# Optimization experiments

Hardware: AMD Instinct MI355X
Metric: run time of the kernel (lower is better)

Reference implementation:

```python
import jax, jax.numpy as jnp
import numpy as np

B, LC, LQ = 16, 512, 64
H = 256            # args.hidden_dim (BiLSTM output dim)
D = 4 * H          # feedforward / biaffine input dim
DFF = 512          # args.hidden_dim_ffw
C = 3              # num_labels


def setup_inputs() -> dict:
    key = jax.random.key(0)
    ks = jax.random.split(key, 12)
    sc = 0.02
    return {
        "ctx_emb": jax.random.normal(ks[0], (B, LC, H), jnp.float32),
        "ques_emb": jax.random.normal(ks[1], (B, LQ, H), jnp.float32),
        "w_sim": jax.random.normal(ks[2], (3 * H,), jnp.float32) * sc,
        "W1s": jax.random.normal(ks[3], (D, DFF), jnp.float32) * sc,
        "b1s": jnp.zeros((DFF,), jnp.float32),
        "W2s": jax.random.normal(ks[4], (DFF, D), jnp.float32) * sc,
        "b2s": jnp.zeros((D,), jnp.float32),
        "W1e": jax.random.normal(ks[5], (D, DFF), jnp.float32) * sc,
        "b1e": jnp.zeros((DFF,), jnp.float32),
        "W2e": jax.random.normal(ks[6], (DFF, D), jnp.float32) * sc,
        "b2e": jnp.zeros((D,), jnp.float32),
        "Wb": jax.random.normal(ks[7], (D + 1, C, D + 1), jnp.float32) * sc,
    }


def _ffw(x, W1, b1, W2, b2):
    # FeedforwardLayer: w_2(relu(w_1(x))) (dropout is identity at eval)
    return jnp.maximum(x @ W1 + b1, 0.0) @ W2 + b2


def reference(ctx_emb, ques_emb, w_sim, W1s, b1s, W2s, b2s, W1e, b1e, W2e, b2e, Wb):
    w1, w2, w3 = jnp.split(w_sim, 3)
    # Fused BiDAF trilinear similarity: identical math to
    # Linear(cat([ctx_, ques_, ctx_*ques_], -1)) with weight [w1|w2|w3].
    sim = (ctx_emb @ w1)[:, :, None] + (ques_emb @ w2)[:, None, :] \
        + jnp.einsum('bih,bjh->bij', ctx_emb * w3, ques_emb)      # [B,LC,LQ]
    a = jax.nn.softmax(sim, axis=-1)                               # [B,LC,LQ]
    c2q = jnp.einsum('bij,bjh->bih', a, ques_emb)                  # [B,LC,H]
    b = jax.nn.softmax(jnp.max(sim, axis=2), axis=-1)              # [B,LC]
    q2c = jnp.einsum('bi,bih->bh', b, ctx_emb)[:, None, :]         # [B,1,H] broadcast over LC
    x = jnp.concatenate([ctx_emb, c2q, ctx_emb * c2q, ctx_emb * q2c], axis=2)  # [B,LC,4H]
    start = _ffw(x, W1s, b1s, W2s, b2s)                            # [B,LC,D]
    end = _ffw(x, W1e, b1e, W2e, b2e)                              # [B,LC,D]
    ones = jnp.ones(start.shape[:-1] + (1,), start.dtype)
    s1 = jnp.concatenate([start, ones], axis=-1)                   # [B,LC,D+1]
    e1 = jnp.concatenate([end, ones], axis=-1)                     # [B,LC,D+1]
    # Biaffine: score[b,x,y,c] = s1[b,x] . Wb[:,c,:] . e1[b,y]
    return jnp.einsum('bxi,icj,byj->bxyc', s1, Wb, e1)             # [B,LC,LC,C]
```

## Files before the change

### kernel.cpp

```cpp
#include <hip/hip_runtime.h>
#include <hip/hip_bf16.h>
#include <math.h>

typedef __bf16 bf16_t;
typedef bf16_t bf16x4 __attribute__((ext_vector_type(4)));
typedef bf16_t bf16x8 __attribute__((ext_vector_type(8)));
typedef float f32x4 __attribute__((ext_vector_type(4)));

#define Bsz 16
#define LCc 512
#define LQq 64
#define Hd 256
#define Dd 1024
#define DFFd 512
#define DP1 1025
#define KP 1152
#define NT 18
#define NIT 9
#define NP 1280
#define NROW 8192
#define YC 1536

#define OFF_T    0L
#define OFF_QW2  0L
#define OFF_MROW 4096L
#define OFF_Q2C  (OFF_MROW + 32768L)
#define OFF_C2Q  (OFF_Q2C + 16384L)
#define OFF_XB   (OFF_C2Q + 8388608L)
#define OFF_HBUF (OFF_XB + 16777216L)
#define OFF_W1ST (OFF_HBUF + 8388608L)
#define OFF_W2ST (OFF_W1ST + 1048576L)
#define OFF_W1ET (OFF_W2ST + 1048576L)
#define OFF_W2ET (OFF_W1ET + 1048576L)
#define OFF_S1   56623104L
#define OFF_E1   (OFF_S1 + 18874368L)
#define OFF_WBT  (OFF_E1 + 18874368L)

static __device__ __forceinline__ void gload_lds16(const void* g, void* l) {
    __builtin_amdgcn_global_load_lds(
        (const __attribute__((address_space(1))) void*)g,
        (__attribute__((address_space(3))) void*)l, 16, 0, 0);
}

__global__ __launch_bounds__(256) void k_qw2(const float* __restrict__ ques,
                                             const float* __restrict__ wsim,
                                             float* __restrict__ qw2) {
    int row = blockIdx.x * 4 + (threadIdx.x >> 6);
    int lane = threadIdx.x & 63;
    float4 q = *(const float4*)&ques[(long)row * Hd + lane * 4];
    float4 w = *(const float4*)&wsim[Hd + lane * 4];
    float p = q.x * w.x + q.y * w.y + q.z * w.z + q.w * w.w;
#pragma unroll
    for (int o = 32; o >= 1; o >>= 1) p += __shfl_xor(p, o, 64);
    if (lane == 0) qw2[row] = p;
}

__global__ __launch_bounds__(256) void k_wtrans(const float* __restrict__ in,
                                                bf16_t* __restrict__ out,
                                                int K, int N) {
    __shared__ float tile[32][33];
    int k0 = blockIdx.x * 32, n0 = blockIdx.y * 32;
    int r = threadIdx.x >> 5, c = threadIdx.x & 31;
#pragma unroll
    for (int rr = 0; rr < 32; rr += 8)
        tile[r + rr][c] = in[(long)(k0 + r + rr) * N + n0 + c];
    __syncthreads();
#pragma unroll
    for (int rr = 0; rr < 32; rr += 8)
        out[(long)(n0 + r + rr) * K + k0 + c] = (bf16_t)tile[c][r + rr];
}

__global__ __launch_bounds__(256) void k_wb(const float* __restrict__ Wb,
                                            bf16_t* __restrict__ Wbt) {
    int rowz = blockIdx.x;
    int c = rowz / NP, i = rowz % NP;
    int tid = threadIdx.x;
    bf16_t* orow = Wbt + (long)rowz * KP;
#pragma unroll
    for (int p = 0; p < 2; p++) {
        int j4 = tid + p * 256;
        if (j4 < KP / 4) {
            int j = j4 * 4;
            float x = 0.f, y = 0.f, z = 0.f, w = 0.f;
            if (i < DP1) {
                const float* src = Wb + ((long)i * 3 + c) * DP1 + j;
                if (j + 0 < DP1) x = src[0];
                if (j + 1 < DP1) y = src[1];
                if (j + 2 < DP1) z = src[2];
                if (j + 3 < DP1) w = src[3];
            }
            bf16x4 bv = {(bf16_t)x, (bf16_t)y, (bf16_t)z, (bf16_t)w};
            *(bf16x4*)&orow[j] = bv;
        }
    }
}

__global__ __launch_bounds__(256) void k_initse(bf16_t* __restrict__ s1,
                                                bf16_t* __restrict__ e1) {
    int idx = blockIdx.x * 256 + threadIdx.x;
    long r = idx >> 7; int cc = idx & 127;
    bf16_t v = (bf16_t)(cc == 0 ? 1.0f : 0.0f);
    s1[r * KP + 1024 + cc] = v;
    e1[r * KP + 1024 + cc] = v;
}

__global__ __launch_bounds__(256) void k_attn(const float* __restrict__ ctx,
                                              const float* __restrict__ ques,
                                              const float* __restrict__ wsim,
                                              const float* __restrict__ qw2,
                                              float* __restrict__ c2q,
                                              float* __restrict__ mrow) {
    __shared__ bf16x4 qlds[LQq * 64];
    __shared__ float cw3s[4][Hd];
    __shared__ float awave[4][LQq];
    int b = blockIdx.x >> 5;
    int itile = blockIdx.x & 31;
    int tid = threadIdx.x, wid = tid >> 6, lane = tid & 63;
#pragma unroll
    for (int p = 0; p < 16; p++) {
        int s = tid + p * 256;
        int j = s >> 6, h4s = s & 63;
        int h4 = h4s ^ (j & 15);
        float4 v = *(const float4*)&ques[((long)b * LQq + j) * Hd + h4 * 4];
        bf16x4 bv = {(bf16_t)v.x, (bf16_t)v.y, (bf16_t)v.z, (bf16_t)v.w};
        qlds[s] = bv;
    }
    float qw2r = qw2[b * LQq + lane];
    float4 w1v = *(const float4*)&wsim[lane * 4];
    float4 w3v = *(const float4*)&wsim[2 * Hd + lane * 4];
    __syncthreads();
    for (int rr = 0; rr < 4; rr++) {
        int i = itile * 16 + wid * 4 + rr;
        float4 cv = *(const float4*)&ctx[((long)b * LCc + i) * Hd + lane * 4];
        float cw1p = cv.x * w1v.x + cv.y * w1v.y + cv.z * w1v.z + cv.w * w1v.w;
        float4 c3;
        c3.x = cv.x * w3v.x; c3.y = cv.y * w3v.y;
        c3.z = cv.z * w3v.z; c3.w = cv.w * w3v.w;
        *(float4*)&cw3s[wid][lane * 4] = c3;
#pragma unroll
        for (int o = 32; o >= 1; o >>= 1) cw1p += __shfl_xor(cw1p, o, 64);
        __syncthreads();
        float s = cw1p + qw2r;
#pragma unroll 8
        for (int h4 = 0; h4 < 64; h4++) {
            float4 c3v = *(const float4*)&cw3s[wid][h4 * 4];
            bf16x4 qb = qlds[lane * 64 + (h4 ^ (lane & 15))];
            s += c3v.x * (float)qb[0] + c3v.y * (float)qb[1]
               + c3v.z * (float)qb[2] + c3v.w * (float)qb[3];
        }
        float mx = s;
#pragma unroll
        for (int o = 32; o >= 1; o >>= 1) mx = fmaxf(mx, __shfl_xor(mx, o, 64));
        if (lane == 0) mrow[b * LCc + i] = mx;
        float pe = __expf(s - mx);
        float den = pe;
#pragma unroll
        for (int o = 32; o >= 1; o >>= 1) den += __shfl_xor(den, o, 64);
        awave[wid][lane] = pe / den;
        __syncthreads();
        float4 accv = {0.f, 0.f, 0.f, 0.f};
#pragma unroll 8
        for (int j = 0; j < 64; j++) {
            float aj = awave[wid][j];
            bf16x4 qb = qlds[j * 64 + (lane ^ (j & 15))];
            accv.x = fmaf(aj, (float)qb[0], accv.x);
            accv.y = fmaf(aj, (float)qb[1], accv.y);
            accv.z = fmaf(aj, (float)qb[2], accv.z);
            accv.w = fmaf(aj, (float)qb[3], accv.w);
        }
        *(float4*)&c2q[((long)b * LCc + i) * Hd + lane * 4] = accv;
        __syncthreads();
    }
}

__global__ __launch_bounds__(256) void k_q2c(const float* __restrict__ ctx,
                                             const float* __restrict__ mrow,
                                             float* __restrict__ q2c) {
    __shared__ float wbuf[LCc];
    __shared__ float red[8];
    int b = blockIdx.x, tid = threadIdx.x;
    float v0 = mrow[b * LCc + tid], v1 = mrow[b * LCc + 256 + tid];
    float m = fmaxf(v0, v1);
#pragma unroll
    for (int o = 32; o >= 1; o >>= 1) m = fmaxf(m, __shfl_xor(m, o, 64));
    if ((tid & 63) == 0) red[tid >> 6] = m;
    __syncthreads();
    float M = fmaxf(fmaxf(red[0], red[1]), fmaxf(red[2], red[3]));
    float e0 = __expf(v0 - M), e1v = __expf(v1 - M);
    float sm = e0 + e1v;
#pragma unroll
    for (int o = 32; o >= 1; o >>= 1) sm += __shfl_xor(sm, o, 64);
    if ((tid & 63) == 0) red[4 + (tid >> 6)] = sm;
    __syncthreads();
    float S = red[4] + red[5] + red[6] + red[7];
    wbuf[tid] = e0 / S;
    wbuf[tid + 256] = e1v / S;
    __syncthreads();
    float acc = 0.f;
#pragma unroll 8
    for (int i = 0; i < LCc; i++)
        acc = fmaf(wbuf[i], ctx[((long)b * LCc + i) * Hd + tid], acc);
    q2c[b * Hd + tid] = acc;
}

__global__ __launch_bounds__(256) void k_buildx(const float* __restrict__ ctx,
                                                const float* __restrict__ c2q,
                                                const float* __restrict__ q2c,
                                                bf16_t* __restrict__ xb) {
    long r = blockIdx.x;
    int b = (int)(r >> 9);
    int tid = threadIdx.x;
    int sec = tid >> 6, h4 = tid & 63;
    float4 cv = *(const float4*)&ctx[r * Hd + h4 * 4];
    float4 v;
    if (sec == 0) {
        v = cv;
    } else if (sec == 1) {
        v = *(const float4*)&c2q[r * Hd + h4 * 4];
    } else if (sec == 2) {
        float4 q = *(const float4*)&c2q[r * Hd + h4 * 4];
        v.x = cv.x * q.x; v.y = cv.y * q.y; v.z = cv.z * q.z; v.w = cv.w * q.w;
    } else {
        float4 q = *(const float4*)&q2c[b * Hd + h4 * 4];
        v.x = cv.x * q.x; v.y = cv.y * q.y; v.z = cv.z * q.z; v.w = cv.w * q.w;
    }
    bf16x4 bv = {(bf16_t)v.x, (bf16_t)v.y, (bf16_t)v.z, (bf16_t)v.w};
    *(bf16x4*)&xb[r * Dd + sec * Hd + h4 * 4] = bv;
}

template <int MODE>
__global__ __launch_bounds__(256, 2) void gemm_nt(
    const bf16_t* __restrict__ A, const bf16_t* __restrict__ B,
    const float* __restrict__ bias, void* __restrict__ C,
    int K, int lda, int ldb) {
    __shared__ bf16_t As[128 * 32];
    __shared__ bf16_t Bs[128 * 32];
    int tid = threadIdx.x;
    int wid = tid >> 6, lane = tid & 63;
    const bf16_t* Ab = A + (long)blockIdx.x * 128 * lda;
    const bf16_t* Bb = B + (long)blockIdx.y * 128 * ldb;
    int wr = (wid >> 1) * 64, wc = (wid & 1) * 64;
    int fr = lane & 15, kg = lane >> 4;
    f32x4 acc[4][4] = {};
    for (int k0 = 0; k0 < K; k0 += 32) {
        __syncthreads();
#pragma unroll
        for (int p = 0; p < 2; p++) {
            int q = tid + p * 256;
            int row = q >> 2, cg = q & 3;
            gload_lds16(Ab + (long)row * lda + k0 + cg * 8, &As[q * 8]);
            gload_lds16(Bb + (long)row * ldb + k0 + cg * 8, &Bs[q * 8]);
        }
        __syncthreads();
        bf16x8 af[4], bq[4];
#pragma unroll
        for (int m = 0; m < 4; m++)
            af[m] = *(const bf16x8*)&As[(wr + m * 16 + fr) * 32 + kg * 8];
#pragma unroll
        for (int n = 0; n < 4; n++)
            bq[n] = *(const bf16x8*)&Bs[(wc + n * 16 + fr) * 32 + kg * 8];
#pragma unroll
        for (int m = 0; m < 4; m++)
#pragma unroll
            for (int n = 0; n < 4; n++)
                acc[m][n] = __builtin_amdgcn_mfma_f32_16x16x32_bf16(
                    af[m], bq[n], acc[m][n], 0, 0, 0);
    }
    int g4 = (lane >> 4) * 4;
#pragma unroll
    for (int m = 0; m < 4; m++) {
#pragma unroll
        for (int g = 0; g < 4; g++) {
            long r = (long)blockIdx.x * 128 + wr + m * 16 + g4 + g;
#pragma unroll
            for (int n = 0; n < 4; n++) {
                int col = blockIdx.y * 128 + wc + n * 16 + fr;
                float v = acc[m][n][g] + bias[col];
                if (MODE == 0) {
                    v = fmaxf(v, 0.f);
                    ((bf16_t*)C)[r * DFFd + col] = (bf16_t)v;
                } else {
                    ((bf16_t*)C)[r * KP + col] = (bf16_t)v;
                }
            }
        }
    }
}

template <int MODE>
__global__ __launch_bounds__(512) void gemm8(
    const bf16_t* __restrict__ A, const bf16_t* __restrict__ B,
    void* __restrict__ C, int nbx, int nby) {
    __shared__ char smem[131072];
    int tid = threadIdx.x;
    const int nz = (MODE == 2) ? 3 : Bsz;
    int nwg = nbx * nby * nz;
    int nper = nwg >> 3;
    int wg = blockIdx.x;
    int wgid = (wg & 7) * nper + (wg >> 3);
    int z = wgid / (nbx * nby);
    int rem = wgid - z * nbx * nby;
    int by = rem / nbx, bx = rem - by * nbx;
    const bf16_t* At;
    const bf16_t* Bt;
    if (MODE == 2) {
        At = A + (long)bx * 256 * KP;
        Bt = B + ((long)z * NP + by * 256) * KP;
    } else {
        At = A + ((long)z * LCc + bx * 256) * KP;
        Bt = B + ((long)z * YC + by * 256) * KP;
    }
    int lane = tid & 63, wv = tid >> 6, wm = wv >> 2, wn = wv & 3;
    int fr = lane & 15, kg = lane >> 4;
    int row0 = tid >> 3, sc0 = (tid & 7) ^ (row0 & 7);
    int q1 = tid + 512;
    int row1 = q1 >> 3, sc1 = (q1 & 7) ^ (row1 & 7);

    auto STAGE = [&](int mat, int ht, int tile) {
        int ts = tile <= NT - 1 ? tile : NT - 1;
        int buf = tile & 1;
        const bf16_t* base = mat ? Bt : At;
        long rb = (long)ht * 128;
        const bf16_t* g0 = base + (rb + row0) * KP + ts * 64 + sc0 * 8;
        const bf16_t* g1 = base + (rb + row1) * KP + ts * 64 + sc1 * 8;
        char* l = smem + (mat ? 65536 : 0) + buf * 32768 + ht * 16384;
        gload_lds16(g0, l + tid * 16);
        gload_lds16(g1, l + 8192 + tid * 16);
    };
    auto RDA = [&](int buf, int h, int m, int kk) -> bf16x8 {
        int row = wm * 128 + h * 64 + m * 16 + fr;
        int c16 = kk * 4 + kg;
        int off = buf * 32768 + row * 128 + ((c16 ^ (row & 7)) << 4);
        return *(const bf16x8*)(smem + off);
    };
    auto RDB = [&](int buf, int v, int n, int kk) -> bf16x8 {
        int row = wn * 64 + v * 32 + n * 16 + fr;
        int c16 = kk * 4 + kg;
        int off = 65536 + buf * 32768 + row * 128 + ((c16 ^ (row & 7)) << 4);
        return *(const bf16x8*)(smem + off);
    };

    f32x4 acc[8][4] = {};

    STAGE(0, 0, 0); STAGE(0, 1, 0); STAGE(1, 0, 0); STAGE(1, 1, 0);
    STAGE(0, 0, 1); STAGE(0, 1, 1);
    asm volatile("s_waitcnt vmcnt(4)" ::: "memory");
    __builtin_amdgcn_s_barrier();

    auto doTile = [&](int buf, int sB, int sA, bool boundary) {
        bf16x8 aL[4][2], aH[4][2], bE[2][2], bO[2][2];
#pragma unroll
        for (int m = 0; m < 4; m++)
#pragma unroll
            for (int k = 0; k < 2; k++) aL[m][k] = RDA(buf, 0, m, k);
#pragma unroll
        for (int n = 0; n < 2; n++)
#pragma unroll
            for (int k = 0; k < 2; k++) bE[n][k] = RDB(buf, 0, n, k);
        STAGE(1, 0, sB);
        __builtin_amdgcn_s_barrier();
        __builtin_amdgcn_s_setprio(1);
#pragma unroll
        for (int m = 0; m < 4; m++)
#pragma unroll
            for (int n = 0; n < 2; n++)
#pragma unroll
                for (int k = 0; k < 2; k++)
                    acc[m][n] = __builtin_amdgcn_mfma_f32_16x16x32_bf16(
                        aL[m][k], bE[n][k], acc[m][n], 0, 0, 0);
        __builtin_amdgcn_s_setprio(0);
        __builtin_amdgcn_s_barrier();
#pragma unroll
        for (int n = 0; n < 2; n++)
#pragma unroll
            for (int k = 0; k < 2; k++) bO[n][k] = RDB(buf, 1, n, k);
        STAGE(1, 1, sB);
        __builtin_amdgcn_s_barrier();
        __builtin_amdgcn_s_setprio(1);
#pragma unroll
        for (int m = 0; m < 4; m++)
#pragma unroll
            for (int n = 0; n < 2; n++)
#pragma unroll
                for (int k = 0; k < 2; k++)
                    acc[m][2 + n] = __builtin_amdgcn_mfma_f32_16x16x32_bf16(
                        aL[m][k], bO[n][k], acc[m][2 + n], 0, 0, 0);
        __builtin_amdgcn_s_setprio(0);
        __builtin_amdgcn_s_barrier();
#pragma unroll
        for (int m = 0; m < 4; m++)
#pragma unroll
            for (int k = 0; k < 2; k++) aH[m][k] = RDA(buf, 1, m, k);
        STAGE(0, 0, sA);
        __builtin_amdgcn_s_barrier();
        __builtin_amdgcn_s_setprio(1);
#pragma unroll
        for (int m = 0; m < 4; m++)
#pragma unroll
            for (int n = 0; n < 2; n++)
#pragma unroll
                for (int k = 0; k < 2; k++)
                    acc[4 + m][n] = __builtin_amdgcn_mfma_f32_16x16x32_bf16(
                        aH[m][k], bE[n][k], acc[4 + m][n], 0, 0, 0);
        __builtin_amdgcn_s_setprio(0);
        __builtin_amdgcn_s_barrier();
        STAGE(0, 1, sA);
        __builtin_amdgcn_s_barrier();
        __builtin_amdgcn_s_setprio(1);
#pragma unroll
        for (int m = 0; m < 4; m++)
#pragma unroll
            for (int n = 0; n < 2; n++)
#pragma unroll
                for (int k = 0; k < 2; k++)
                    acc[4 + m][2 + n] = __builtin_amdgcn_mfma_f32_16x16x32_bf16(
                        aH[m][k], bO[n][k], acc[4 + m][2 + n], 0, 0, 0);
        __builtin_amdgcn_s_setprio(0);
        asm volatile("s_waitcnt vmcnt(4)" ::: "memory");
        __builtin_amdgcn_s_barrier();
        (void)boundary;
    };

    for (int it = 0; it < NIT; ++it) {
        int t = 2 * it;
        doTile(0, t + 1, t + 2, false);
        doTile(1, t + 2, t + 3, true);
    }

#pragma unroll
    for (int mf = 0; mf < 8; mf++) {
#pragma unroll
        for (int g = 0; g < 4; g++) {
            long r = (long)bx * 256 + wm * 128 + mf * 16 + kg * 4 + g;
#pragma unroll
            for (int nf = 0; nf < 4; nf++) {
                int col = by * 256 + wn * 64 + nf * 16 + fr;
                float v = acc[mf][nf][g];
                if (MODE == 2) {
                    if (col < KP)
                        ((bf16_t*)C)[(r * 3 + z) * (long)KP + col] = (bf16_t)v;
                } else {
                    ((float*)C)[(long)z * (LCc * YC) + r * YC + col] = v;
                }
            }
        }
    }
}

extern "C" void kernel_launch(void* const* d_in, const int* in_sizes, int n_in,
                              void* d_out, int out_size, void* d_ws, size_t ws_size,
                              hipStream_t stream) {
    const float* ctx  = (const float*)d_in[0];
    const float* ques = (const float*)d_in[1];
    const float* wsim = (const float*)d_in[2];
    const float* W1s  = (const float*)d_in[3];
    const float* b1s  = (const float*)d_in[4];
    const float* W2s  = (const float*)d_in[5];
    const float* b2s  = (const float*)d_in[6];
    const float* W1e  = (const float*)d_in[7];
    const float* b1e  = (const float*)d_in[8];
    const float* W2e  = (const float*)d_in[9];
    const float* b2e  = (const float*)d_in[10];
    const float* Wb   = (const float*)d_in[11];

    char* ws = (char*)d_ws;
    float*  qw2  = (float*)(ws + OFF_QW2);
    float*  mrow = (float*)(ws + OFF_MROW);
    float*  q2c  = (float*)(ws + OFF_Q2C);
    float*  c2q  = (float*)(ws + OFF_C2Q);
    bf16_t* xb   = (bf16_t*)(ws + OFF_XB);
    bf16_t* hbuf = (bf16_t*)(ws + OFF_HBUF);
    bf16_t* W1st = (bf16_t*)(ws + OFF_W1ST);
    bf16_t* W2st = (bf16_t*)(ws + OFF_W2ST);
    bf16_t* W1et = (bf16_t*)(ws + OFF_W1ET);
    bf16_t* W2et = (bf16_t*)(ws + OFF_W2ET);
    bf16_t* T    = (bf16_t*)(ws + OFF_T);
    bf16_t* s1   = (bf16_t*)(ws + OFF_S1);
    bf16_t* e1   = (bf16_t*)(ws + OFF_E1);
    bf16_t* Wbt  = (bf16_t*)(ws + OFF_WBT);

    k_qw2<<<256, 256, 0, stream>>>(ques, wsim, qw2);
    k_wtrans<<<dim3(32, 16), 256, 0, stream>>>(W1s, W1st, 1024, 512);
    k_wtrans<<<dim3(16, 32), 256, 0, stream>>>(W2s, W2st, 512, 1024);
    k_wtrans<<<dim3(32, 16), 256, 0, stream>>>(W1e, W1et, 1024, 512);
    k_wtrans<<<dim3(16, 32), 256, 0, stream>>>(W2e, W2et, 512, 1024);
    k_wb<<<3 * NP, 256, 0, stream>>>(Wb, Wbt);
    k_attn<<<Bsz * 32, 256, 0, stream>>>(ctx, ques, wsim, qw2, c2q, mrow);
    k_q2c<<<Bsz, 256, 0, stream>>>(ctx, mrow, q2c);
    k_buildx<<<NROW, 256, 0, stream>>>(ctx, c2q, q2c, xb);
    k_initse<<<4096, 256, 0, stream>>>(s1, e1);

    gemm_nt<0><<<dim3(64, 4), 256, 0, stream>>>(xb, W1st, b1s, hbuf, 1024, 1024, 1024);
    gemm_nt<1><<<dim3(64, 8), 256, 0, stream>>>(hbuf, W2st, b2s, s1, 512, 512, 512);
    gemm_nt<0><<<dim3(64, 4), 256, 0, stream>>>(xb, W1et, b1e, hbuf, 1024, 1024, 1024);
    gemm_nt<1><<<dim3(64, 8), 256, 0, stream>>>(hbuf, W2et, b2e, e1, 512, 512, 512);
    gemm8<2><<<480, 512, 0, stream>>>(e1, Wbt, T, 32, 5);
    gemm8<3><<<192, 512, 0, stream>>>(s1, T, d_out, 2, 6);
}
```

Measured before the change: 358.6 us.

## Merge start/end FFN GEMMs, trim biaffine padding, split q2c reduction

The start and end feedforward branches are concatenated: W1 for both branches is stacked into one 1024-wide GEMM, and W2 runs as one batched launch with blockIdx.z selecting the branch. The biaffine first GEMM drops the padded i-dimension (1280 to 1024 rows) and computes the bias row i=1024 of T in a separate small k_gcol kernel. q2c is parallelized over 128 blocks with a partial-sum reduction instead of 16 blocks. Together these cut launches and remove wasted padded MFMA work, at the cost of more index arithmetic and an extra small kernel.

```diff
diff --git a/kernel.cpp b/kernel.cpp
--- a/kernel.cpp
+++ b/kernel.cpp
@@ -15,26 +15,22 @@
 #define DFFd 512
 #define DP1 1025
 #define KP 1152
-#define NT 18
-#define NIT 9
-#define NP 1280
+#define NTT 18
 #define NROW 8192
 #define YC 1536
 
 #define OFF_T    0L
 #define OFF_QW2  0L
 #define OFF_MROW 4096L
-#define OFF_Q2C  (OFF_MROW + 32768L)
-#define OFF_C2Q  (OFF_Q2C + 16384L)
-#define OFF_XB   (OFF_C2Q + 8388608L)
-#define OFF_HBUF (OFF_XB + 16777216L)
-#define OFF_W1ST (OFF_HBUF + 8388608L)
-#define OFF_W2ST (OFF_W1ST + 1048576L)
-#define OFF_W1ET (OFF_W2ST + 1048576L)
-#define OFF_W2ET (OFF_W1ET + 1048576L)
+#define OFF_Q2C  36864L
+#define OFF_C2Q  53248L
+#define OFF_XB   8441856L
+#define OFF_HBUF 25219072L
+#define OFF_W1C  41996288L
+#define OFF_W2C  44093440L
 #define OFF_S1   56623104L
-#define OFF_E1   (OFF_S1 + 18874368L)
-#define OFF_WBT  (OFF_E1 + 18874368L)
+#define OFF_E1   75497472L
+#define OFF_WBT  94371840L
 
 static __device__ __forceinline__ void gload_lds16(const void* g, void* l) {
     __builtin_amdgcn_global_load_lds(
@@ -72,23 +68,20 @@
 
 __global__ __launch_bounds__(256) void k_wb(const float* __restrict__ Wb,
                                             bf16_t* __restrict__ Wbt) {
-    int rowz = blockIdx.x;
-    int c = rowz / NP, i = rowz % NP;
+    int rw = blockIdx.x;
+    int c = rw >> 10, i = rw & 1023;
     int tid = threadIdx.x;
-    bf16_t* orow = Wbt + (long)rowz * KP;
+    const float* src = Wb + ((long)i * 3 + c) * DP1;
+    bf16_t* orow = Wbt + (long)rw * KP;
 #pragma unroll
     for (int p = 0; p < 2; p++) {
         int j4 = tid + p * 256;
         if (j4 < KP / 4) {
             int j = j4 * 4;
-            float x = 0.f, y = 0.f, z = 0.f, w = 0.f;
-            if (i < DP1) {
-                const float* src = Wb + ((long)i * 3 + c) * DP1 + j;
-                if (j + 0 < DP1) x = src[0];
-                if (j + 1 < DP1) y = src[1];
-                if (j + 2 < DP1) z = src[2];
-                if (j + 3 < DP1) w = src[3];
-            }
+            float x = (j + 0 < DP1) ? src[j + 0] : 0.f;
+            float y = (j + 1 < DP1) ? src[j + 1] : 0.f;
+            float z = (j + 2 < DP1) ? src[j + 2] : 0.f;
+            float w = (j + 3 < DP1) ? src[j + 3] : 0.f;
             bf16x4 bv = {(bf16_t)x, (bf16_t)y, (bf16_t)z, (bf16_t)w};
             *(bf16x4*)&orow[j] = bv;
         }
@@ -178,7 +171,10 @@
                                              float* __restrict__ q2c) {
     __shared__ float wbuf[LCc];
     __shared__ float red[8];
-    int b = blockIdx.x, tid = threadIdx.x;
+    __shared__ float part[8][32];
+    int blk = blockIdx.x;
+    int b = blk >> 3, hc = blk & 7;
+    int tid = threadIdx.x;
     float v0 = mrow[b * LCc + tid], v1 = mrow[b * LCc + 256 + tid];
     float m = fmaxf(v0, v1);
 #pragma unroll
@@ -196,11 +192,22 @@
     wbuf[tid] = e0 / S;
     wbuf[tid + 256] = e1v / S;
     __syncthreads();
+    int ig = tid >> 5, h31 = tid & 31;
+    int h = hc * 32 + h31;
     float acc = 0.f;
-#pragma unroll 8
-    for (int i = 0; i < LCc; i++)
-        acc = fmaf(wbuf[i], ctx[((long)b * LCc + i) * Hd + tid], acc);
-    q2c[b * Hd + tid] = acc;
+#pragma unroll 4
+    for (int ii = 0; ii < 64; ii++) {
+        int i = ig * 64 + ii;
+        acc = fmaf(wbuf[i], ctx[((long)b * LCc + i) * Hd + h], acc);
+    }
+    part[ig][h31] = acc;
+    __syncthreads();
+    if (tid < 32) {
+        float s = 0.f;
+#pragma unroll
+        for (int k = 0; k < 8; k++) s += part[k][tid];
+        q2c[b * Hd + hc * 32 + tid] = s;
+    }
 }
 
 __global__ __launch_bounds__(256) void k_buildx(const float* __restrict__ ctx,
@@ -228,17 +235,49 @@
     *(bf16x4*)&xb[r * Dd + sec * Hd + h4 * 4] = bv;
 }
 
+__global__ __launch_bounds__(256) void k_gcol(const bf16_t* __restrict__ e1,
+                                              const float* __restrict__ Wb,
+                                              bf16_t* __restrict__ T) {
+    int tid = threadIdx.x;
+    int wv = tid >> 6, lane = tid & 63;
+    long r = (long)blockIdx.x * 4 + wv;
+    bf16x8 ea = *(const bf16x8*)&e1[r * KP + lane * 16];
+    bf16x8 eb = *(const bf16x8*)&e1[r * KP + lane * 16 + 8];
+    const float* wr0 = Wb + (long)3072 * DP1;
+#pragma unroll
+    for (int c = 0; c < 3; c++) {
+        const float* wr = wr0 + (long)c * DP1 + lane * 16;
+        float acc = 0.f;
+#pragma unroll
+        for (int k = 0; k < 8; k++) {
+            acc = fmaf((float)ea[k], wr[k], acc);
+            acc = fmaf((float)eb[k], wr[8 + k], acc);
+        }
+#pragma unroll
+        for (int o = 32; o >= 1; o >>= 1) acc += __shfl_xor(acc, o, 64);
+        long rowb = (r * 3 + c) * (long)KP;
+        if (lane == 0)
+            T[rowb + 1024] = (bf16_t)(acc + wr0[(long)c * DP1 + 1024]);
+        for (int jj = 1025 + lane; jj < KP; jj += 64)
+            T[rowb + jj] = (bf16_t)0.f;
+    }
+}
+
 template <int MODE>
 __global__ __launch_bounds__(256, 2) void gemm_nt(
     const bf16_t* __restrict__ A, const bf16_t* __restrict__ B,
-    const float* __restrict__ bias, void* __restrict__ C,
-    int K, int lda, int ldb) {
+    const float* __restrict__ bias0, const float* __restrict__ bias1,
+    bf16_t* __restrict__ C0, bf16_t* __restrict__ C1) {
+    const int K = (MODE == 0) ? 1024 : 512;
+    const int lda = 1024;
+    const int ldb = (MODE == 0) ? 1024 : 512;
     __shared__ bf16_t As[128 * 32];
     __shared__ bf16_t Bs[128 * 32];
     int tid = threadIdx.x;
     int wid = tid >> 6, lane = tid & 63;
-    const bf16_t* Ab = A + (long)blockIdx.x * 128 * lda;
-    const bf16_t* Bb = B + (long)blockIdx.y * 128 * ldb;
+    int z = (MODE == 1) ? blockIdx.z : 0;
+    const bf16_t* Ab = A + (long)blockIdx.x * 128 * lda + z * 512;
+    const bf16_t* Bb = B + (long)z * 1024 * 512 + (long)blockIdx.y * 128 * ldb;
     int wr = (wid >> 1) * 64, wc = (wid & 1) * 64;
     int fr = lane & 15, kg = lane >> 4;
     f32x4 acc[4][4] = {};
@@ -275,12 +314,14 @@
 #pragma unroll
             for (int n = 0; n < 4; n++) {
                 int col = blockIdx.y * 128 + wc + n * 16 + fr;
-                float v = acc[m][n][g] + bias[col];
+                float v = acc[m][n][g];
                 if (MODE == 0) {
+                    v += (col < 512) ? bias0[col] : bias1[col - 512];
                     v = fmaxf(v, 0.f);
-                    ((bf16_t*)C)[r * DFFd + col] = (bf16_t)v;
+                    C0[r * 1024 + col] = (bf16_t)v;
                 } else {
-                    ((bf16_t*)C)[r * KP + col] = (bf16_t)v;
+                    v += z ? bias1[col] : bias0[col];
+                    (z ? C1 : C0)[r * (long)KP + col] = (bf16_t)v;
                 }
             }
         }
@@ -290,26 +331,29 @@
 template <int MODE>
 __global__ __launch_bounds__(512) void gemm8(
     const bf16_t* __restrict__ A, const bf16_t* __restrict__ B,
-    void* __restrict__ C, int nbx, int nby) {
+    void* __restrict__ C) {
     __shared__ char smem[131072];
     int tid = threadIdx.x;
-    const int nz = (MODE == 2) ? 3 : Bsz;
-    int nwg = nbx * nby * nz;
-    int nper = nwg >> 3;
     int wg = blockIdx.x;
-    int wgid = (wg & 7) * nper + (wg >> 3);
-    int z = wgid / (nbx * nby);
-    int rem = wgid - z * nbx * nby;
-    int by = rem / nbx, bx = rem - by * nbx;
-    const bf16_t* At;
-    const bf16_t* Bt;
+    int bx, zz, yy;
     if (MODE == 2) {
-        At = A + (long)bx * 256 * KP;
-        Bt = B + ((long)z * NP + by * 256) * KP;
+        int wgid = (wg & 7) * 48 + (wg >> 3);
+        int wi = wgid & 15, st = wgid >> 4;
+        bx = (st & 7) * 4 + (wi & 3);
+        int byN = (st >> 3) * 4 + (wi >> 2);
+        zz = byN >> 2; yy = byN & 3;
     } else {
-        At = A + ((long)z * LCc + bx * 256) * KP;
-        Bt = B + ((long)z * YC + by * 256) * KP;
-    }
+        int wgid = (wg & 7) * 24 + (wg >> 3);
+        bx = wgid & 1;
+        int byz = wgid >> 1;
+        zz = byz / 6; yy = byz % 6;
+    }
+    long Aoff = (MODE == 2) ? (long)bx * 256 * KP
+                            : ((long)zz * 512 + bx * 256) * KP;
+    long Boff = (MODE == 2) ? (long)(zz * 4 + yy) * 256 * KP
+                            : ((long)zz * 1536 + yy * 256) * KP;
+    const bf16_t* At = A + Aoff;
+    const bf16_t* Bt = B + Boff;
     int lane = tid & 63, wv = tid >> 6, wm = wv >> 2, wn = wv & 3;
     int fr = lane & 15, kg = lane >> 4;
     int row0 = tid >> 3, sc0 = (tid & 7) ^ (row0 & 7);
@@ -317,7 +361,7 @@
     int row1 = q1 >> 3, sc1 = (q1 & 7) ^ (row1 & 7);
 
     auto STAGE = [&](int mat, int ht, int tile) {
-        int ts = tile <= NT - 1 ? tile : NT - 1;
+        int ts = tile <= NTT - 1 ? tile : NTT - 1;
         int buf = tile & 1;
         const bf16_t* base = mat ? Bt : At;
         long rb = (long)ht * 128;
@@ -347,7 +391,7 @@
     asm volatile("s_waitcnt vmcnt(4)" ::: "memory");
     __builtin_amdgcn_s_barrier();
 
-    auto doTile = [&](int buf, int sB, int sA, bool boundary) {
+    auto doTile = [&](int buf, int sB, int sA) {
         bf16x8 aL[4][2], aH[4][2], bE[2][2], bO[2][2];
 #pragma unroll
         for (int m = 0; m < 4; m++)
@@ -418,29 +462,29 @@
         __builtin_amdgcn_s_setprio(0);
         asm volatile("s_waitcnt vmcnt(4)" ::: "memory");
         __builtin_amdgcn_s_barrier();
-        (void)boundary;
     };
 
-    for (int it = 0; it < NIT; ++it) {
+    for (int it = 0; it < NTT / 2; ++it) {
         int t = 2 * it;
-        doTile(0, t + 1, t + 2, false);
-        doTile(1, t + 2, t + 3, true);
+        doTile(0, t + 1, t + 2);
+        doTile(1, t + 2, t + 3);
     }
 
 #pragma unroll
     for (int mf = 0; mf < 8; mf++) {
 #pragma unroll
         for (int g = 0; g < 4; g++) {
-            long r = (long)bx * 256 + wm * 128 + mf * 16 + kg * 4 + g;
+            int rloc = wm * 128 + mf * 16 + kg * 4 + g;
 #pragma unroll
             for (int nf = 0; nf < 4; nf++) {
-                int col = by * 256 + wn * 64 + nf * 16 + fr;
+                int col = wn * 64 + nf * 16 + fr;
                 float v = acc[mf][nf][g];
                 if (MODE == 2) {
-                    if (col < KP)
-                        ((bf16_t*)C)[(r * 3 + z) * (long)KP + col] = (bf16_t)v;
+                    long r = (long)bx * 256 + rloc;
+                    ((bf16_t*)C)[(r * 3 + zz) * (long)KP + yy * 256 + col] = (bf16_t)v;
                 } else {
-                    ((float*)C)[(long)z * (LCc * YC) + r * YC + col] = v;
+                    long r = (long)bx * 256 + rloc;
+                    ((float*)C)[(long)zz * (512L * YC) + r * YC + yy * 256 + col] = v;
                 }
             }
         }
@@ -470,30 +514,27 @@
     float*  c2q  = (float*)(ws + OFF_C2Q);
     bf16_t* xb   = (bf16_t*)(ws + OFF_XB);
     bf16_t* hbuf = (bf16_t*)(ws + OFF_HBUF);
-    bf16_t* W1st = (bf16_t*)(ws + OFF_W1ST);
-    bf16_t* W2st = (bf16_t*)(ws + OFF_W2ST);
-    bf16_t* W1et = (bf16_t*)(ws + OFF_W1ET);
-    bf16_t* W2et = (bf16_t*)(ws + OFF_W2ET);
+    bf16_t* W1c  = (bf16_t*)(ws + OFF_W1C);
+    bf16_t* W2c  = (bf16_t*)(ws + OFF_W2C);
     bf16_t* T    = (bf16_t*)(ws + OFF_T);
     bf16_t* s1   = (bf16_t*)(ws + OFF_S1);
     bf16_t* e1   = (bf16_t*)(ws + OFF_E1);
     bf16_t* Wbt  = (bf16_t*)(ws + OFF_WBT);
 
     k_qw2<<<256, 256, 0, stream>>>(ques, wsim, qw2);
-    k_wtrans<<<dim3(32, 16), 256, 0, stream>>>(W1s, W1st, 1024, 512);
-    k_wtrans<<<dim3(16, 32), 256, 0, stream>>>(W2s, W2st, 512, 1024);
-    k_wtrans<<<dim3(32, 16), 256, 0, stream>>>(W1e, W1et, 1024, 512);
-    k_wtrans<<<dim3(16, 32), 256, 0, stream>>>(W2e, W2et, 512, 1024);
-    k_wb<<<3 * NP, 256, 0, stream>>>(Wb, Wbt);
+    k_wtrans<<<dim3(32, 16), 256, 0, stream>>>(W1s, W1c, 1024, 512);
+    k_wtrans<<<dim3(32, 16), 256, 0, stream>>>(W1e, W1c + 512 * 1024, 1024, 512);
+    k_wtrans<<<dim3(16, 32), 256, 0, stream>>>(W2s, W2c, 512, 1024);
+    k_wtrans<<<dim3(16, 32), 256, 0, stream>>>(W2e, W2c + 1024 * 512, 512, 1024);
+    k_wb<<<3072, 256, 0, stream>>>(Wb, Wbt);
     k_attn<<<Bsz * 32, 256, 0, stream>>>(ctx, ques, wsim, qw2, c2q, mrow);
-    k_q2c<<<Bsz, 256, 0, stream>>>(ctx, mrow, q2c);
+    k_q2c<<<128, 256, 0, stream>>>(ctx, mrow, q2c);
     k_buildx<<<NROW, 256, 0, stream>>>(ctx, c2q, q2c, xb);
     k_initse<<<4096, 256, 0, stream>>>(s1, e1);
 
-    gemm_nt<0><<<dim3(64, 4), 256, 0, stream>>>(xb, W1st, b1s, hbuf, 1024, 1024, 1024);
-    gemm_nt<1><<<dim3(64, 8), 256, 0, stream>>>(hbuf, W2st, b2s, s1, 512, 512, 512);
-    gemm_nt<0><<<dim3(64, 4), 256, 0, stream>>>(xb, W1et, b1e, hbuf, 1024, 1024, 1024);
-    gemm_nt<1><<<dim3(64, 8), 256, 0, stream>>>(hbuf, W2et, b2e, e1, 512, 512, 512);
-    gemm8<2><<<480, 512, 0, stream>>>(e1, Wbt, T, 32, 5);
-    gemm8<3><<<192, 512, 0, stream>>>(s1, T, d_out, 2, 6);
-}
+    gemm_nt<0><<<dim3(64, 8), 256, 0, stream>>>(xb, W1c, b1s, b1e, hbuf, nullptr);
+    gemm_nt<1><<<dim3(64, 8, 2), 256, 0, stream>>>(hbuf, W2c, b2s, b2e, s1, e1);
+    k_gcol<<<2048, 256, 0, stream>>>(e1, Wb, T);
+    gemm8<2><<<384, 512, 0, stream>>>(e1, Wbt, T);
+    gemm8<3><<<192, 512, 0, stream>>>(s1, T, d_out);
+}
```

Result: faster. 314.7 us (-12.2%).
